# Optimization experiments

Measured on AMD Instinct MI355X. Metric: run time of the kernel, lower is better.

Reference implementation:

```python
import jax, jax.numpy as jnp
import numpy as np

N_NODES = 50000
N_EDGES = 800000
IN_CH, HID_CH, OUT_CH = 128, 128, 64


def setup_inputs() -> dict:
    key = jax.random.key(0)
    ks = jax.random.split(key, 8)
    x = jax.random.normal(ks[0], (N_NODES, IN_CH), dtype=jnp.float32)
    src = jax.random.randint(ks[1], (N_EDGES,), 0, N_NODES, dtype=jnp.int32)
    dst = jax.random.randint(ks[2], (N_EDGES,), 0, N_NODES, dtype=jnp.int32)
    s1 = 1.0 / np.sqrt(IN_CH)
    s2 = 1.0 / np.sqrt(HID_CH)
    W_self1 = jax.random.normal(ks[3], (IN_CH, HID_CH), dtype=jnp.float32) * s1
    W_neigh1 = jax.random.normal(ks[4], (IN_CH, HID_CH), dtype=jnp.float32) * s1
    b1 = jnp.zeros((HID_CH,), dtype=jnp.float32)
    W_self2 = jax.random.normal(ks[5], (HID_CH, OUT_CH), dtype=jnp.float32) * s2
    W_neigh2 = jax.random.normal(ks[6], (HID_CH, OUT_CH), dtype=jnp.float32) * s2
    b2 = jnp.zeros((OUT_CH,), dtype=jnp.float32)
    return {"x": x, "src": src, "dst": dst,
            "W_self1": W_self1, "W_neigh1": W_neigh1, "b1": b1,
            "W_self2": W_self2, "W_neigh2": W_neigh2, "b2": b2}


def _mean_agg(h, src, dst, inv_deg):
    # gather source features, scatter-sum onto destinations, divide by in-degree
    summed = jax.ops.segment_sum(h[src], dst, num_segments=N_NODES)  # [N, d]
    return summed * inv_deg[:, None]


def _sage_layer(h, src, dst, inv_deg, W_self, W_neigh, b):
    h_neigh = _mean_agg(h, src, dst, inv_deg)
    return h @ W_self + h_neigh @ W_neigh + b


def reference(x, src, dst, W_self1, W_neigh1, b1, W_self2, W_neigh2, b2):
    deg = jax.ops.segment_sum(jnp.ones_like(dst, dtype=x.dtype), dst,
                              num_segments=N_NODES)
    inv_deg = 1.0 / jnp.maximum(deg, 1.0)  # isolated nodes -> 0 neighbor feature
    h = _sage_layer(x, src, dst, inv_deg, W_self1, W_neigh1, b1)
    h = jax.nn.relu(h)
    out = _sage_layer(h, src, dst, inv_deg, W_self2, W_neigh2, b2)
    return out
```

## Files before the change

### kernel.cpp

```cpp
#include <hip/hip_runtime.h>

#define N_CH 128
#define CAP 7680

typedef short bf16x8 __attribute__((ext_vector_type(8)));
typedef float f32x4 __attribute__((ext_vector_type(4)));

__device__ __forceinline__ unsigned short f2bf(float f) {
    unsigned int u = __float_as_uint(f);
    unsigned int r = (u + 0x7fffu + ((u >> 16) & 1u)) >> 16;
    return (unsigned short)r;
}
__device__ __forceinline__ unsigned int pkbf(float a, float b) {
    return (unsigned int)f2bf(a) | ((unsigned int)f2bf(b) << 16);
}
__device__ __forceinline__ float bflo(unsigned int v) { return __uint_as_float(v << 16); }
__device__ __forceinline__ float bfhi(unsigned int v) { return __uint_as_float(v & 0xffff0000u); }

__global__ __launch_bounds__(256) void k_inithist(const float* __restrict__ Ws1,
                                                  const float* __restrict__ Wn1,
                                                  const float* __restrict__ Ws2,
                                                  const float* __restrict__ Wn2,
                                                  unsigned short* __restrict__ Bt1,
                                                  unsigned short* __restrict__ Bt2,
                                                  const int* __restrict__ dst,
                                                  int* __restrict__ H, int e, int nbh,
                                                  int nbkt) {
    __shared__ int hist[256];
    int b = blockIdx.x, t = threadIdx.x;
    if (b < 192) {
        int idx = b * 256 + t;
        if (idx < 128 * 256) {
            int n = idx >> 8, k = idx & 255;
            float v = (k < 128) ? Ws1[k * 128 + n] : Wn1[(k - 128) * 128 + n];
            Bt1[idx] = f2bf(v);
        } else {
            int j = idx - 128 * 256;
            int n = j >> 7, k = j & 127;
            float v = (n < 64) ? Ws2[k * 64 + n] : Wn2[k * 64 + (n - 64)];
            Bt2[j] = f2bf(v);
        }
    } else {
        int hb = b - 192;
        hist[t] = 0;
        __syncthreads();
        int i = hb * 1024 + t * 4;
        if (i + 3 < e) {
            int4 d4 = *(const int4*)&dst[i];
            atomicAdd(&hist[d4.x >> 8], 1);
            atomicAdd(&hist[d4.y >> 8], 1);
            atomicAdd(&hist[d4.z >> 8], 1);
            atomicAdd(&hist[d4.w >> 8], 1);
        } else {
            for (int j = i; j < e && j < i + 4; ++j) atomicAdd(&hist[dst[j] >> 8], 1);
        }
        __syncthreads();
        if (t < nbkt) H[t * nbh + hb] = hist[t];
    }
}

__global__ __launch_bounds__(256) void k_reduce(const int* __restrict__ H,
                                                int* __restrict__ bsum, int tot) {
    __shared__ int sm[256];
    int i = blockIdx.x * 256 + threadIdx.x;
    sm[threadIdx.x] = (i < tot) ? H[i] : 0;
    __syncthreads();
    for (int s = 128; s > 0; s >>= 1) {
        if (threadIdx.x < s) sm[threadIdx.x] += sm[threadIdx.x + s];
        __syncthreads();
    }
    if (threadIdx.x == 0) bsum[blockIdx.x] = sm[0];
}

__global__ __launch_bounds__(256) void k_scan(const int* __restrict__ H,
                                              const int* __restrict__ bsum,
                                              int* __restrict__ Hs, int tot) {
    __shared__ int sm[256];
    __shared__ int sbase;
    int t = threadIdx.x, b = blockIdx.x;
    int acc = 0;
    for (int j = t; j < b; j += 256) acc += bsum[j];
    sm[t] = acc;
    __syncthreads();
    for (int s = 128; s > 0; s >>= 1) {
        if (t < s) sm[t] += sm[t + s];
        __syncthreads();
    }
    if (t == 0) sbase = sm[0];
    __syncthreads();
    int base = sbase;
    __syncthreads();
    int i = b * 256 + t;
    int v = (i < tot) ? H[i] : 0;
    sm[t] = v;
    __syncthreads();
    for (int off = 1; off < 256; off <<= 1) {
        int add = (t >= off) ? sm[t - off] : 0;
        __syncthreads();
        sm[t] += add;
        __syncthreads();
    }
    if (i < tot) Hs[i] = base + sm[t] - v;
}

__global__ __launch_bounds__(256) void k_scatcast(const int* __restrict__ src,
                                                  const int* __restrict__ dst,
                                                  const int* __restrict__ Hs,
                                                  int* __restrict__ buf,
                                                  int e, int nbh, int nbkt,
                                                  const float* __restrict__ x,
                                                  uint4* __restrict__ xb4, int nxq) {
    __shared__ int cur[256];
    int t = threadIdx.x, b = blockIdx.x;
    if (b < nbh) {
        if (t < nbkt) cur[t] = Hs[t * nbh + b];
        __syncthreads();
        int i = b * 1024 + t * 4;
        if (i + 3 < e) {
            int4 d4 = *(const int4*)&dst[i];
            int4 s4 = *(const int4*)&src[i];
            int r0 = atomicAdd(&cur[d4.x >> 8], 1);
            buf[r0] = ((d4.x & 255) << 16) | s4.x;
            int r1 = atomicAdd(&cur[d4.y >> 8], 1);
            buf[r1] = ((d4.y & 255) << 16) | s4.y;
            int r2 = atomicAdd(&cur[d4.z >> 8], 1);
            buf[r2] = ((d4.z & 255) << 16) | s4.z;
            int r3 = atomicAdd(&cur[d4.w >> 8], 1);
            buf[r3] = ((d4.w & 255) << 16) | s4.w;
        } else {
            for (int j = i; j < e && j < i + 4; ++j) {
                int d = dst[j];
                int r = atomicAdd(&cur[d >> 8], 1);
                buf[r] = ((d & 255) << 16) | src[j];
            }
        }
    } else {
        int q = (b - nbh) * 256 + t;
        if (q < nxq) {
            const float4* xf = (const float4*)x;
            float4 f0 = xf[2 * q], f1 = xf[2 * q + 1];
            uint4 o;
            o.x = pkbf(f0.x, f0.y); o.y = pkbf(f0.z, f0.w);
            o.z = pkbf(f1.x, f1.y); o.w = pkbf(f1.z, f1.w);
            xb4[q] = o;
        }
    }
}

__global__ __launch_bounds__(256) void k_bucket(const int* __restrict__ buf,
                                                const int* __restrict__ Hs,
                                                unsigned short* __restrict__ csr_src,
                                                int* __restrict__ deg,
                                                int* __restrict__ row_start,
                                                int e, int nbh, int nbkt, int n) {
    __shared__ int hist[256];
    __shared__ int excl[256];
    __shared__ int cur[256];
    __shared__ int cache[CAP];
    int t = threadIdx.x, b = blockIdx.x;
    int base = Hs[b * nbh];
    int end = (b == nbkt - 1) ? e : Hs[(b + 1) * nbh];
    int cnt = end - base;
    hist[t] = 0;
    __syncthreads();
    for (int i = t; i < cnt; i += 256) {
        int v = buf[base + i];
        if (i < CAP) cache[i] = v;
        atomicAdd(&hist[(v >> 16) & 255], 1);
    }
    __syncthreads();
    int v = hist[t];
    excl[t] = v;
    __syncthreads();
    for (int off = 1; off < 256; off <<= 1) {
        int add = (t >= off) ? excl[t - off] : 0;
        __syncthreads();
        excl[t] += add;
        __syncthreads();
    }
    int ex = excl[t] - v;
    cur[t] = ex;
    int node = b * 256 + t;
    if (node < n) {
        deg[node] = v;
        row_start[node] = base + ex;
    }
    __syncthreads();
    for (int i = t; i < cnt; i += 256) {
        int ed = (i < CAP) ? cache[i] : buf[base + i];
        int r = atomicAdd(&cur[(ed >> 16) & 255], 1);
        csr_src[base + r] = (unsigned short)(ed & 0xFFFF);
    }
}

__global__ __launch_bounds__(256) void k_aggx(const uint4* __restrict__ xb4,
                                              uint4* __restrict__ xagg4,
                                              const int* __restrict__ row_start,
                                              const int* __restrict__ deg,
                                              const unsigned short* __restrict__ csr, int n) {
    int gw = (blockIdx.x * 256 + threadIdx.x) >> 6;
    int lane = threadIdx.x & 63;
    if (gw >= n) return;
    int start = row_start[gw];
    int cnt = deg[gw];
    const int q = lane >> 4;
    const int cl = lane & 15;
    float a0 = 0.f, a1 = 0.f, a2 = 0.f, a3 = 0.f, a4 = 0.f, a5 = 0.f, a6 = 0.f, a7 = 0.f;
    int i = 0;
    for (; i + 16 <= cnt; i += 16) {
        int e0 = csr[start + i + q];
        int e1 = csr[start + i + 4 + q];
        int e2 = csr[start + i + 8 + q];
        int e3 = csr[start + i + 12 + q];
        uint4 v0 = xb4[e0 * 16 + cl];
        uint4 v1 = xb4[e1 * 16 + cl];
        uint4 v2 = xb4[e2 * 16 + cl];
        uint4 v3 = xb4[e3 * 16 + cl];
        a0 += bflo(v0.x) + bflo(v1.x) + bflo(v2.x) + bflo(v3.x);
        a1 += bfhi(v0.x) + bfhi(v1.x) + bfhi(v2.x) + bfhi(v3.x);
        a2 += bflo(v0.y) + bflo(v1.y) + bflo(v2.y) + bflo(v3.y);
        a3 += bfhi(v0.y) + bfhi(v1.y) + bfhi(v2.y) + bfhi(v3.y);
        a4 += bflo(v0.z) + bflo(v1.z) + bflo(v2.z) + bflo(v3.z);
        a5 += bfhi(v0.z) + bfhi(v1.z) + bfhi(v2.z) + bfhi(v3.z);
        a6 += bflo(v0.w) + bflo(v1.w) + bflo(v2.w) + bflo(v3.w);
        a7 += bfhi(v0.w) + bfhi(v1.w) + bfhi(v2.w) + bfhi(v3.w);
    }
    if (i + 8 <= cnt) {
        int e0 = csr[start + i + q];
        int e1 = csr[start + i + 4 + q];
        uint4 v0 = xb4[e0 * 16 + cl];
        uint4 v1 = xb4[e1 * 16 + cl];
        a0 += bflo(v0.x) + bflo(v1.x); a1 += bfhi(v0.x) + bfhi(v1.x);
        a2 += bflo(v0.y) + bflo(v1.y); a3 += bfhi(v0.y) + bfhi(v1.y);
        a4 += bflo(v0.z) + bflo(v1.z); a5 += bfhi(v0.z) + bfhi(v1.z);
        a6 += bflo(v0.w) + bflo(v1.w); a7 += bfhi(v0.w) + bfhi(v1.w);
        i += 8;
    }
    for (; i < cnt; i += 4) {
        int nbi = i + q;
        if (nbi < cnt) {
            uint4 va = xb4[csr[start + nbi] * 16 + cl];
            a0 += bflo(va.x); a1 += bfhi(va.x);
            a2 += bflo(va.y); a3 += bfhi(va.y);
            a4 += bflo(va.z); a5 += bfhi(va.z);
            a6 += bflo(va.w); a7 += bfhi(va.w);
        }
    }
    a0 += __shfl_xor(a0, 16); a0 += __shfl_xor(a0, 32);
    a1 += __shfl_xor(a1, 16); a1 += __shfl_xor(a1, 32);
    a2 += __shfl_xor(a2, 16); a2 += __shfl_xor(a2, 32);
    a3 += __shfl_xor(a3, 16); a3 += __shfl_xor(a3, 32);
    a4 += __shfl_xor(a4, 16); a4 += __shfl_xor(a4, 32);
    a5 += __shfl_xor(a5, 16); a5 += __shfl_xor(a5, 32);
    a6 += __shfl_xor(a6, 16); a6 += __shfl_xor(a6, 32);
    a7 += __shfl_xor(a7, 16); a7 += __shfl_xor(a7, 32);

    float inv = 1.0f / fmaxf((float)cnt, 1.0f);
    if (q == 0) {
        uint4 o;
        o.x = pkbf(inv * a0, inv * a1);
        o.y = pkbf(inv * a2, inv * a3);
        o.z = pkbf(inv * a4, inv * a5);
        o.w = pkbf(inv * a6, inv * a7);
        xagg4[gw * 16 + cl] = o;
    }
}

__global__ __launch_bounds__(256) void k_gemm12(const uint4* __restrict__ xb4,
                                                const uint4* __restrict__ xagg4,
                                                const unsigned short* __restrict__ Bt1,
                                                const float* __restrict__ b1,
                                                const unsigned short* __restrict__ Bt2,
                                                const float* __restrict__ b2,
                                                float* __restrict__ out,
                                                unsigned short* __restrict__ p2, int M) {
    __shared__ unsigned short As[64][256];
    unsigned short* lds = &As[0][0];
    const int m0 = blockIdx.x * 64;
    const int tid = threadIdx.x;
    const int w = tid >> 6;
    const int l = tid & 63;
    const int fr = l & 15;
    const int kq = l >> 4;

    for (int p = tid; p < 2048; p += 256) {
        int row = p >> 5, c = p & 31;
        int gr = m0 + row;
        uint4 v = make_uint4(0, 0, 0, 0);
        if (gr < M) v = (c < 16) ? xb4[gr * 16 + c] : xagg4[gr * 16 + (c - 16)];
        *(uint4*)&As[row][(c ^ (row & 7)) * 8] = v;
    }
    __syncthreads();

    f32x4 acc[2][4] = {};
#pragma unroll
    for (int kt = 0; kt < 8; ++kt) {
        bf16x8 bfr[2];
#pragma unroll
        for (int ct = 0; ct < 2; ++ct) {
            int nn = w * 32 + ct * 16 + fr;
            bfr[ct] = *(const bf16x8*)&Bt1[nn * 256 + kt * 32 + kq * 8];
        }
        bf16x8 af[4];
#pragma unroll
        for (int rt = 0; rt < 4; ++rt) {
            int row = rt * 16 + fr;
            int c = (kt * 4 + kq) ^ (row & 7);
            af[rt] = *(bf16x8*)&As[row][c * 8];
        }
#pragma unroll
        for (int ct = 0; ct < 2; ++ct)
#pragma unroll
            for (int rt = 0; rt < 4; ++rt)
                acc[ct][rt] = __builtin_amdgcn_mfma_f32_16x16x32_bf16(af[rt], bfr[ct],
                                                                      acc[ct][rt], 0, 0, 0);
    }
    __syncthreads();

#pragma unroll
    for (int ct = 0; ct < 2; ++ct) {
        int col = w * 32 + ct * 16 + fr;
        float bv = b1[col];
        int c8 = col >> 3, c7 = col & 7;
#pragma unroll
        for (int rt = 0; rt < 4; ++rt) {
#pragma unroll
            for (int j = 0; j < 4; ++j) {
                int row = rt * 16 + (l >> 4) * 4 + j;
                unsigned short hv = f2bf(fmaxf(acc[ct][rt][j] + bv, 0.f));
                lds[row * 128 + (c8 ^ (row & 7)) * 8 + c7] = hv;
            }
        }
    }
    __syncthreads();

    f32x4 acc2[2][4] = {};
#pragma unroll
    for (int kt = 0; kt < 4; ++kt) {
        bf16x8 bfr[2];
#pragma unroll
        for (int ct = 0; ct < 2; ++ct) {
            int nn = w * 32 + ct * 16 + fr;
            bfr[ct] = *(const bf16x8*)&Bt2[nn * 128 + kt * 32 + kq * 8];
        }
        bf16x8 af[4];
#pragma unroll
        for (int rt = 0; rt < 4; ++rt) {
            int row = rt * 16 + fr;
            int c = (kt * 4 + kq) ^ (row & 7);
            af[rt] = *(bf16x8*)&lds[row * 128 + c * 8];
        }
#pragma unroll
        for (int ct = 0; ct < 2; ++ct)
#pragma unroll
            for (int rt = 0; rt < 4; ++rt)
                acc2[ct][rt] = __builtin_amdgcn_mfma_f32_16x16x32_bf16(af[rt], bfr[ct],
                                                                       acc2[ct][rt], 0, 0, 0);
    }

#pragma unroll
    for (int ct = 0; ct < 2; ++ct) {
        int col = w * 32 + ct * 16 + fr;
        bool isS = col < 64;
        float bv = isS ? b2[col] : 0.f;
#pragma unroll
        for (int rt = 0; rt < 4; ++rt) {
#pragma unroll
            for (int j = 0; j < 4; ++j) {
                int row = m0 + rt * 16 + (l >> 4) * 4 + j;
                if (row < M) {
                    float v = acc2[ct][rt][j];
                    if (isS) out[row * 64 + col] = v + bv;
                    else p2[row * 64 + (col - 64)] = f2bf(v);
                }
            }
        }
    }
}

__global__ __launch_bounds__(256) void k_agg2_add(const unsigned int* __restrict__ p,
                                                  float* __restrict__ out,
                                                  const int* __restrict__ row_start,
                                                  const int* __restrict__ deg,
                                                  const unsigned short* __restrict__ csr,
                                                  int n) {
    int gw = (blockIdx.x * 256 + threadIdx.x) >> 6;
    int lane = threadIdx.x & 63;
    if (gw >= n) return;
    int start = row_start[gw];
    int cnt = deg[gw];
    const int g = lane >> 3;
    const int cl = lane & 7;
    float a0 = 0.f, a1 = 0.f, a2 = 0.f, a3 = 0.f, a4 = 0.f, a5 = 0.f, a6 = 0.f, a7 = 0.f;
    int i = 0;
    for (; i + 16 <= cnt; i += 16) {
        int e0 = csr[start + i + g];
        int e1 = csr[start + i + 8 + g];
        uint4 v0 = *(const uint4*)&p[e0 * 32 + cl * 4];
        uint4 v1 = *(const uint4*)&p[e1 * 32 + cl * 4];
        a0 += bflo(v0.x) + bflo(v1.x); a1 += bfhi(v0.x) + bfhi(v1.x);
        a2 += bflo(v0.y) + bflo(v1.y); a3 += bfhi(v0.y) + bfhi(v1.y);
        a4 += bflo(v0.z) + bflo(v1.z); a5 += bfhi(v0.z) + bfhi(v1.z);
        a6 += bflo(v0.w) + bflo(v1.w); a7 += bfhi(v0.w) + bfhi(v1.w);
    }
    for (; i < cnt; i += 8) {
        int nbi = i + g;
        if (nbi < cnt) {
            int ia = csr[start + nbi];
            uint4 va = *(const uint4*)&p[ia * 32 + cl * 4];
            a0 += bflo(va.x); a1 += bfhi(va.x);
            a2 += bflo(va.y); a3 += bfhi(va.y);
            a4 += bflo(va.z); a5 += bfhi(va.z);
            a6 += bflo(va.w); a7 += bfhi(va.w);
        }
    }
    a0 += __shfl_xor(a0, 8); a0 += __shfl_xor(a0, 16); a0 += __shfl_xor(a0, 32);
    a1 += __shfl_xor(a1, 8); a1 += __shfl_xor(a1, 16); a1 += __shfl_xor(a1, 32);
    a2 += __shfl_xor(a2, 8); a2 += __shfl_xor(a2, 16); a2 += __shfl_xor(a2, 32);
    a3 += __shfl_xor(a3, 8); a3 += __shfl_xor(a3, 16); a3 += __shfl_xor(a3, 32);
    a4 += __shfl_xor(a4, 8); a4 += __shfl_xor(a4, 16); a4 += __shfl_xor(a4, 32);
    a5 += __shfl_xor(a5, 8); a5 += __shfl_xor(a5, 16); a5 += __shfl_xor(a5, 32);
    a6 += __shfl_xor(a6, 8); a6 += __shfl_xor(a6, 16); a6 += __shfl_xor(a6, 32);
    a7 += __shfl_xor(a7, 8); a7 += __shfl_xor(a7, 16); a7 += __shfl_xor(a7, 32);
    float inv = 1.0f / fmaxf((float)cnt, 1.0f);
    if (g == 0) {
        float4 oa = *(const float4*)&out[gw * 64 + cl * 8];
        float4 ob = *(const float4*)&out[gw * 64 + cl * 8 + 4];
        oa.x += inv * a0; oa.y += inv * a1; oa.z += inv * a2; oa.w += inv * a3;
        ob.x += inv * a4; ob.y += inv * a5; ob.z += inv * a6; ob.w += inv * a7;
        *(float4*)&out[gw * 64 + cl * 8] = oa;
        *(float4*)&out[gw * 64 + cl * 8 + 4] = ob;
    }
}

extern "C" void kernel_launch(void* const* d_in, const int* in_sizes, int n_in,
                              void* d_out, int out_size, void* d_ws, size_t ws_size,
                              hipStream_t stream) {
    const float* x   = (const float*)d_in[0];
    const int*   src = (const int*)d_in[1];
    const int*   dst = (const int*)d_in[2];
    const float* Ws1 = (const float*)d_in[3];
    const float* Wn1 = (const float*)d_in[4];
    const float* b1  = (const float*)d_in[5];
    const float* Ws2 = (const float*)d_in[6];
    const float* Wn2 = (const float*)d_in[7];
    const float* b2  = (const float*)d_in[8];
    float* out = (float*)d_out;
    const int N = in_sizes[0] / N_CH;
    const int E = in_sizes[1];

    const int nbh  = (E + 1023) / 1024;
    const int nbkt = (N + 255) / 256;
    const int htot = nbkt * nbh;
    const int nb2  = (htot + 255) / 256;
    const int nxq  = N * 16;
    const int nxb  = (nxq + 255) / 256;

    char* ws = (char*)d_ws;
    int* deg       = (int*)(ws + 0);
    int* row_start = (int*)(ws + 200704);
    int* bsum2     = (int*)(ws + 401408);
    unsigned short* csr_src = (unsigned short*)(ws + 403968);
    int* H         = (int*)(ws + 2003968);
    int* Hs        = (int*)(ws + 2617344);
    int* buf       = (int*)(ws + 3230720);
    unsigned short* xb   = (unsigned short*)(ws + 6430720);
    unsigned short* xagg = (unsigned short*)(ws + 19230720);
    unsigned short* p2   = (unsigned short*)(ws + 32030720);
    unsigned short* Bt1  = (unsigned short*)(ws + 38430720);
    unsigned short* Bt2  = (unsigned short*)(ws + 38496256);

    k_inithist<<<192 + nbh, 256, 0, stream>>>(Ws1, Wn1, Ws2, Wn2, Bt1, Bt2, dst, H, E, nbh,
                                              nbkt);
    k_reduce<<<nb2, 256, 0, stream>>>(H, bsum2, htot);
    k_scan<<<nb2, 256, 0, stream>>>(H, bsum2, Hs, htot);
    k_scatcast<<<nbh + nxb, 256, 0, stream>>>(src, dst, Hs, buf, E, nbh, nbkt, x, (uint4*)xb,
                                              nxq);
    k_bucket<<<nbkt, 256, 0, stream>>>(buf, Hs, csr_src, deg, row_start, E, nbh, nbkt, N);

    k_aggx<<<(N + 3) / 4, 256, 0, stream>>>((const uint4*)xb, (uint4*)xagg, row_start, deg,
                                            csr_src, N);

    const int gb = (N + 63) / 64;
    k_gemm12<<<gb, 256, 0, stream>>>((const uint4*)xb, (const uint4*)xagg, Bt1, b1, Bt2, b2,
                                     out, p2, N);
    k_agg2_add<<<(N + 3) / 4, 256, 0, stream>>>((const unsigned int*)p2, out, row_start, deg,
                                                csr_src, N);
}
```

Measured before the change: 112.4 us.

## Move weight and x casts into the bucket kernel to balance kernel loads

Moves the weight transpose/cast blocks out of the histogram kernel and the x-to-bf16 cast blocks out of the scatter kernel, appending both to the bucket-sort kernel's grid. The aim is to keep the histogram and scatter kernels lean and to fill the small bucket kernel (only ~196 blocks) with independent work. The cost is that the cast blocks now share a kernel whose blocks each reserve about 30KB of shared memory for the cache, which could limit occupancy for the cast work.

```diff
diff --git a/kernel.cpp b/kernel.cpp
--- a/kernel.cpp
+++ b/kernel.cpp
@@ -17,46 +17,25 @@
 __device__ __forceinline__ float bflo(unsigned int v) { return __uint_as_float(v << 16); }
 __device__ __forceinline__ float bfhi(unsigned int v) { return __uint_as_float(v & 0xffff0000u); }
 
-__global__ __launch_bounds__(256) void k_inithist(const float* __restrict__ Ws1,
-                                                  const float* __restrict__ Wn1,
-                                                  const float* __restrict__ Ws2,
-                                                  const float* __restrict__ Wn2,
-                                                  unsigned short* __restrict__ Bt1,
-                                                  unsigned short* __restrict__ Bt2,
-                                                  const int* __restrict__ dst,
-                                                  int* __restrict__ H, int e, int nbh,
-                                                  int nbkt) {
+__global__ __launch_bounds__(256) void k_hist(const int* __restrict__ dst,
+                                              int* __restrict__ H, int e, int nbh,
+                                              int nbkt) {
     __shared__ int hist[256];
-    int b = blockIdx.x, t = threadIdx.x;
-    if (b < 192) {
-        int idx = b * 256 + t;
-        if (idx < 128 * 256) {
-            int n = idx >> 8, k = idx & 255;
-            float v = (k < 128) ? Ws1[k * 128 + n] : Wn1[(k - 128) * 128 + n];
-            Bt1[idx] = f2bf(v);
-        } else {
-            int j = idx - 128 * 256;
-            int n = j >> 7, k = j & 127;
-            float v = (n < 64) ? Ws2[k * 64 + n] : Wn2[k * 64 + (n - 64)];
-            Bt2[j] = f2bf(v);
-        }
+    int t = threadIdx.x, hb = blockIdx.x;
+    hist[t] = 0;
+    __syncthreads();
+    int i = hb * 1024 + t * 4;
+    if (i + 3 < e) {
+        int4 d4 = *(const int4*)&dst[i];
+        atomicAdd(&hist[d4.x >> 8], 1);
+        atomicAdd(&hist[d4.y >> 8], 1);
+        atomicAdd(&hist[d4.z >> 8], 1);
+        atomicAdd(&hist[d4.w >> 8], 1);
     } else {
-        int hb = b - 192;
-        hist[t] = 0;
-        __syncthreads();
-        int i = hb * 1024 + t * 4;
-        if (i + 3 < e) {
-            int4 d4 = *(const int4*)&dst[i];
-            atomicAdd(&hist[d4.x >> 8], 1);
-            atomicAdd(&hist[d4.y >> 8], 1);
-            atomicAdd(&hist[d4.z >> 8], 1);
-            atomicAdd(&hist[d4.w >> 8], 1);
-        } else {
-            for (int j = i; j < e && j < i + 4; ++j) atomicAdd(&hist[dst[j] >> 8], 1);
-        }
-        __syncthreads();
-        if (t < nbkt) H[t * nbh + hb] = hist[t];
-    }
+        for (int j = i; j < e && j < i + 4; ++j) atomicAdd(&hist[dst[j] >> 8], 1);
+    }
+    __syncthreads();
+    if (t < nbkt) H[t * nbh + hb] = hist[t];
 }
 
 __global__ __launch_bounds__(256) void k_reduce(const int* __restrict__ H,
@@ -103,39 +82,103 @@
     if (i < tot) Hs[i] = base + sm[t] - v;
 }
 
-__global__ __launch_bounds__(256) void k_scatcast(const int* __restrict__ src,
-                                                  const int* __restrict__ dst,
-                                                  const int* __restrict__ Hs,
-                                                  int* __restrict__ buf,
-                                                  int e, int nbh, int nbkt,
-                                                  const float* __restrict__ x,
-                                                  uint4* __restrict__ xb4, int nxq) {
+__global__ __launch_bounds__(256) void k_scatter(const int* __restrict__ src,
+                                                 const int* __restrict__ dst,
+                                                 const int* __restrict__ Hs,
+                                                 int* __restrict__ buf,
+                                                 int e, int nbh, int nbkt) {
     __shared__ int cur[256];
     int t = threadIdx.x, b = blockIdx.x;
-    if (b < nbh) {
-        if (t < nbkt) cur[t] = Hs[t * nbh + b];
-        __syncthreads();
-        int i = b * 1024 + t * 4;
-        if (i + 3 < e) {
-            int4 d4 = *(const int4*)&dst[i];
-            int4 s4 = *(const int4*)&src[i];
-            int r0 = atomicAdd(&cur[d4.x >> 8], 1);
-            buf[r0] = ((d4.x & 255) << 16) | s4.x;
-            int r1 = atomicAdd(&cur[d4.y >> 8], 1);
-            buf[r1] = ((d4.y & 255) << 16) | s4.y;
-            int r2 = atomicAdd(&cur[d4.z >> 8], 1);
-            buf[r2] = ((d4.z & 255) << 16) | s4.z;
-            int r3 = atomicAdd(&cur[d4.w >> 8], 1);
-            buf[r3] = ((d4.w & 255) << 16) | s4.w;
+    if (t < nbkt) cur[t] = Hs[t * nbh + b];
+    __syncthreads();
+    int i = b * 1024 + t * 4;
+    if (i + 3 < e) {
+        int4 d4 = *(const int4*)&dst[i];
+        int4 s4 = *(const int4*)&src[i];
+        int r0 = atomicAdd(&cur[d4.x >> 8], 1);
+        buf[r0] = ((d4.x & 255) << 16) | s4.x;
+        int r1 = atomicAdd(&cur[d4.y >> 8], 1);
+        buf[r1] = ((d4.y & 255) << 16) | s4.y;
+        int r2 = atomicAdd(&cur[d4.z >> 8], 1);
+        buf[r2] = ((d4.z & 255) << 16) | s4.z;
+        int r3 = atomicAdd(&cur[d4.w >> 8], 1);
+        buf[r3] = ((d4.w & 255) << 16) | s4.w;
+    } else {
+        for (int j = i; j < e && j < i + 4; ++j) {
+            int d = dst[j];
+            int r = atomicAdd(&cur[d >> 8], 1);
+            buf[r] = ((d & 255) << 16) | src[j];
+        }
+    }
+}
+
+__global__ __launch_bounds__(256) void k_bucketcastw(const int* __restrict__ buf,
+                                                     const int* __restrict__ Hs,
+                                                     unsigned short* __restrict__ csr_src,
+                                                     int* __restrict__ deg,
+                                                     int* __restrict__ row_start,
+                                                     int e, int nbh, int nbkt, int n,
+                                                     const float* __restrict__ x,
+                                                     uint4* __restrict__ xb4, int nxq,
+                                                     const float* __restrict__ Ws1,
+                                                     const float* __restrict__ Wn1,
+                                                     const float* __restrict__ Ws2,
+                                                     const float* __restrict__ Wn2,
+                                                     unsigned short* __restrict__ Bt1,
+                                                     unsigned short* __restrict__ Bt2) {
+    __shared__ int hist[256];
+    __shared__ int excl[256];
+    __shared__ int cur[256];
+    __shared__ int cache[CAP];
+    int t = threadIdx.x, b = blockIdx.x;
+    if (b < nbkt) {
+        int base = Hs[b * nbh];
+        int end = (b == nbkt - 1) ? e : Hs[(b + 1) * nbh];
+        int cnt = end - base;
+        hist[t] = 0;
+        __syncthreads();
+        for (int i = t; i < cnt; i += 256) {
+            int v = buf[base + i];
+            if (i < CAP) cache[i] = v;
+            atomicAdd(&hist[(v >> 16) & 255], 1);
+        }
+        __syncthreads();
+        int v = hist[t];
+        excl[t] = v;
+        __syncthreads();
+        for (int off = 1; off < 256; off <<= 1) {
+            int add = (t >= off) ? excl[t - off] : 0;
+            __syncthreads();
+            excl[t] += add;
+            __syncthreads();
+        }
+        int ex = excl[t] - v;
+        cur[t] = ex;
+        int node = b * 256 + t;
+        if (node < n) {
+            deg[node] = v;
+            row_start[node] = base + ex;
+        }
+        __syncthreads();
+        for (int i = t; i < cnt; i += 256) {
+            int ed = (i < CAP) ? cache[i] : buf[base + i];
+            int r = atomicAdd(&cur[(ed >> 16) & 255], 1);
+            csr_src[base + r] = (unsigned short)(ed & 0xFFFF);
+        }
+    } else if (b < nbkt + 192) {
+        int idx = (b - nbkt) * 256 + t;
+        if (idx < 128 * 256) {
+            int nn = idx >> 8, k = idx & 255;
+            float v = (k < 128) ? Ws1[k * 128 + nn] : Wn1[(k - 128) * 128 + nn];
+            Bt1[idx] = f2bf(v);
         } else {
-            for (int j = i; j < e && j < i + 4; ++j) {
-                int d = dst[j];
-                int r = atomicAdd(&cur[d >> 8], 1);
-                buf[r] = ((d & 255) << 16) | src[j];
-            }
+            int j = idx - 128 * 256;
+            int nn = j >> 7, k = j & 127;
+            float v = (nn < 64) ? Ws2[k * 64 + nn] : Wn2[k * 64 + (nn - 64)];
+            Bt2[j] = f2bf(v);
         }
     } else {
-        int q = (b - nbh) * 256 + t;
+        int q = (b - nbkt - 192) * 256 + t;
         if (q < nxq) {
             const float4* xf = (const float4*)x;
             float4 f0 = xf[2 * q], f1 = xf[2 * q + 1];
@@ -144,52 +187,6 @@
             o.z = pkbf(f1.x, f1.y); o.w = pkbf(f1.z, f1.w);
             xb4[q] = o;
         }
-    }
-}
-
-__global__ __launch_bounds__(256) void k_bucket(const int* __restrict__ buf,
-                                                const int* __restrict__ Hs,
-                                                unsigned short* __restrict__ csr_src,
-                                                int* __restrict__ deg,
-                                                int* __restrict__ row_start,
-                                                int e, int nbh, int nbkt, int n) {
-    __shared__ int hist[256];
-    __shared__ int excl[256];
-    __shared__ int cur[256];
-    __shared__ int cache[CAP];
-    int t = threadIdx.x, b = blockIdx.x;
-    int base = Hs[b * nbh];
-    int end = (b == nbkt - 1) ? e : Hs[(b + 1) * nbh];
-    int cnt = end - base;
-    hist[t] = 0;
-    __syncthreads();
-    for (int i = t; i < cnt; i += 256) {
-        int v = buf[base + i];
-        if (i < CAP) cache[i] = v;
-        atomicAdd(&hist[(v >> 16) & 255], 1);
-    }
-    __syncthreads();
-    int v = hist[t];
-    excl[t] = v;
-    __syncthreads();
-    for (int off = 1; off < 256; off <<= 1) {
-        int add = (t >= off) ? excl[t - off] : 0;
-        __syncthreads();
-        excl[t] += add;
-        __syncthreads();
-    }
-    int ex = excl[t] - v;
-    cur[t] = ex;
-    int node = b * 256 + t;
-    if (node < n) {
-        deg[node] = v;
-        row_start[node] = base + ex;
-    }
-    __syncthreads();
-    for (int i = t; i < cnt; i += 256) {
-        int ed = (i < CAP) ? cache[i] : buf[base + i];
-        int r = atomicAdd(&cur[(ed >> 16) & 255], 1);
-        csr_src[base + r] = (unsigned short)(ed & 0xFFFF);
     }
 }
 
@@ -470,13 +467,13 @@
     unsigned short* Bt1  = (unsigned short*)(ws + 38430720);
     unsigned short* Bt2  = (unsigned short*)(ws + 38496256);
 
-    k_inithist<<<192 + nbh, 256, 0, stream>>>(Ws1, Wn1, Ws2, Wn2, Bt1, Bt2, dst, H, E, nbh,
-                                              nbkt);
+    k_hist<<<nbh, 256, 0, stream>>>(dst, H, E, nbh, nbkt);
     k_reduce<<<nb2, 256, 0, stream>>>(H, bsum2, htot);
     k_scan<<<nb2, 256, 0, stream>>>(H, bsum2, Hs, htot);
-    k_scatcast<<<nbh + nxb, 256, 0, stream>>>(src, dst, Hs, buf, E, nbh, nbkt, x, (uint4*)xb,
-                                              nxq);
-    k_bucket<<<nbkt, 256, 0, stream>>>(buf, Hs, csr_src, deg, row_start, E, nbh, nbkt, N);
+    k_scatter<<<nbh, 256, 0, stream>>>(src, dst, Hs, buf, E, nbh, nbkt);
+    k_bucketcastw<<<nbkt + 192 + nxb, 256, 0, stream>>>(buf, Hs, csr_src, deg, row_start,
+                                                        E, nbh, nbkt, N, x, (uint4*)xb, nxq,
+                                                        Ws1, Wn1, Ws2, Wn2, Bt1, Bt2);
 
     k_aggx<<<(N + 3) / 4, 256, 0, stream>>>((const uint4*)xb, (uint4*)xagg, row_start, deg,
                                             csr_src, N);
```

New measurement: 111.3 us. Within noise of the previous version (-1.0%).
